# Kernel optimization log

Measured on AMD Instinct MI355X. Metric: run time of the kernel, lower is better.

## Reference

```python
import jax, jax.numpy as jnp
import numpy as np

N_HEAD = 16

def setup_inputs() -> dict:
    key = jax.random.key(0)
    k1, k2, k3 = jax.random.split(key, 3)
    B, T, C = 4, 2048, 1024
    x = jax.random.normal(k1, (B, T, C), dtype=jnp.float32)
    w_attn = jax.random.normal(k2, (C, 3 * C), dtype=jnp.float32) * (1.0 / np.sqrt(C))
    w_proj = jax.random.normal(k3, (C, C), dtype=jnp.float32) * (1.0 / np.sqrt(C))
    return {"x": x, "w_attn": w_attn, "w_proj": w_proj}

def reference(x, w_attn, w_proj):
    B, T, C = x.shape
    H = N_HEAD
    D = C // H
    qkv = x @ w_attn  # [B, T, 3C]
    q, k, v = jnp.split(qkv, 3, axis=2)
    # [B, H, T, D]
    q = q.reshape(B, T, H, D).transpose(0, 2, 1, 3)
    k = k.reshape(B, T, H, D).transpose(0, 2, 1, 3)
    v = v.reshape(B, T, H, D).transpose(0, 2, 1, 3)
    att = jnp.einsum('bhqd,bhkd->bhqk', q, k) * (1.0 / np.sqrt(D))
    causal = jnp.tril(jnp.ones((T, T), dtype=bool))
    att = jnp.where(causal[None, None, :, :], att, -jnp.inf)
    att = jax.nn.softmax(att, axis=-1)
    y = jnp.einsum('bhqk,bhkd->bhqd', att, v)  # [B, H, T, D]
    y = y.transpose(0, 2, 1, 3).reshape(B, T, C)
    return y @ w_proj
```

## Files before the change

### kernel.cpp

```cpp
#include <hip/hip_runtime.h>
#include <hip/hip_bf16.h>
#include <math.h>

#define B_   4
#define T_   2048
#define C_   1024
#define H_   16
#define D_   64
#define M_   (B_*T_)
#define N3   (3*C_)
#define KDIM C_

typedef __attribute__((ext_vector_type(8)))  short bf16x8;
typedef __attribute__((ext_vector_type(4)))  float f32x4;
typedef __attribute__((ext_vector_type(16))) float f32x16;
typedef __attribute__((ext_vector_type(4)))  unsigned int u32x4;

#define MFMA16(a,b,c) __builtin_amdgcn_mfma_f32_16x16x32_bf16(a,b,c,0,0,0)
#define MFMA32(a,b,c) __builtin_amdgcn_mfma_f32_32x32x16_bf16(a,b,c,0,0,0)

#define QSCALE 0.18033688011112042f

__device__ __forceinline__ unsigned short f2bf(float f) {
  union { float f; unsigned u; } a; a.f = f;
  unsigned r = a.u + 0x7fffu + ((a.u >> 16) & 1u);
  return (unsigned short)(r >> 16);
}

__device__ __forceinline__ unsigned cvtpk(float lo, float hi) {
  unsigned r;
  asm("v_cvt_pk_bf16_f32 %0, %1, %2" : "=v"(r) : "v"(lo), "v"(hi));
  return r;
}

__device__ __forceinline__ void gload16(const void* g, void* l) {
  __builtin_amdgcn_global_load_lds(
      (const __attribute__((address_space(1))) void*)g,
      (__attribute__((address_space(3))) void*)l, 16, 0, 0);
}

__global__ void cast_f32_bf16(const float* __restrict__ in,
                              unsigned short* __restrict__ out, int n) {
  int i = (blockIdx.x * 256 + threadIdx.x) * 4;
  if (i >= n) return;
  float4 v = *(const float4*)(in + i);
  ushort4 o;
  o.x = f2bf(v.x); o.y = f2bf(v.y); o.z = f2bf(v.z); o.w = f2bf(v.w);
  *(ushort4*)(out + i) = o;
}

__global__ void transpose_cast(const float* __restrict__ in,
                               unsigned short* __restrict__ out,
                               int R, int Ncols) {
  __shared__ float tile[32][33];
  int bc = blockIdx.x * 32;
  int br = blockIdx.y * 32;
  int tx = threadIdx.x, ty = threadIdx.y;
  #pragma unroll
  for (int i = ty; i < 32; i += 8)
    tile[i][tx] = in[(size_t)(br + i) * Ncols + bc + tx];
  __syncthreads();
  #pragma unroll
  for (int i = ty; i < 32; i += 8)
    out[(size_t)(bc + i) * R + br + tx] = f2bf(tile[tx][i]);
}

template<int MODE>
__global__ __launch_bounds__(256)
void gemm128(const unsigned short* __restrict__ A,
             const unsigned short* __restrict__ Bt,
             unsigned short* __restrict__ qo,
             unsigned short* __restrict__ ko,
             unsigned short* __restrict__ vto,
             float* __restrict__ outf) {
  __shared__ short Asl[128 * 64];
  __shared__ short Bsl[128 * 64];
  const int tid  = threadIdx.x;
  const int wid  = tid >> 6, lane = tid & 63;
  const int l15  = lane & 15, l4 = lane >> 4;
  const int tm   = blockIdx.y * 128;
  const int tn   = blockIdx.x * 128;
  const int wm   = (wid >> 1) * 64, wn = (wid & 1) * 64;

  f32x4 acc[4][4] = {};
  const int stoff = wid * 1024 + lane * 16;

  for (int kt = 0; kt < KDIM; kt += 64) {
    __syncthreads();
    #pragma unroll
    for (int ro = 0; ro < 4; ++ro) {
      int off = ro * 4096 + stoff;
      int row = off >> 7;
      int ce  = (off & 127) >> 1;
      gload16(A  + (size_t)(tm + row) * KDIM + kt + ce,
              (char*)Asl + ro * 4096 + wid * 1024);
      gload16(Bt + (size_t)(tn + row) * KDIM + kt + ce,
              (char*)Bsl + ro * 4096 + wid * 1024);
    }
    __syncthreads();

    #pragma unroll
    for (int ks = 0; ks < 2; ++ks) {
      bf16x8 af[4], bfr[4];
      #pragma unroll
      for (int i = 0; i < 4; ++i) {
        af[i]  = *(const bf16x8*)&Asl[(wm + i*16 + l15) * 64 + ks*32 + l4*8];
        bfr[i] = *(const bf16x8*)&Bsl[(wn + i*16 + l15) * 64 + ks*32 + l4*8];
      }
      #pragma unroll
      for (int mi = 0; mi < 4; ++mi)
        #pragma unroll
        for (int ni = 0; ni < 4; ++ni)
          acc[mi][ni] = MFMA16(af[mi], bfr[ni], acc[mi][ni]);
    }
  }

  #pragma unroll
  for (int mi = 0; mi < 4; ++mi) {
    #pragma unroll
    for (int ni = 0; ni < 4; ++ni) {
      #pragma unroll
      for (int r = 0; r < 4; ++r) {
        int m = tm + wm + mi*16 + l4*4 + r;
        int n = tn + wn + ni*16 + l15;
        float val = acc[mi][ni][r];
        if (MODE == 0) {
          int b = m >> 11, t = m & (T_ - 1);
          int which = n >> 10, n1 = n & (C_ - 1);
          int h = n1 >> 6, d = n1 & 63;
          size_t bh = (size_t)(b * H_ + h);
          if (which == 0)      qo[(bh * T_ + t) * D_ + d] = f2bf(val * QSCALE);
          else if (which == 1) ko[(bh * T_ + t) * D_ + d] = f2bf(val);
          else                 vto[(bh * D_ + d) * T_ + t] = f2bf(val);
        } else {
          outf[(size_t)m * C_ + n] = val;
        }
      }
    }
  }
}

__global__ __launch_bounds__(256)
void attn32(const unsigned short* __restrict__ Q,
            const unsigned short* __restrict__ K,
            const unsigned short* __restrict__ Vt,
            unsigned short* __restrict__ Y) {
  const int bh   = blockIdx.x;
  const int pair = blockIdx.y;
  const int lane = threadIdx.x & 63, w = threadIdx.x >> 6;
  const int l31  = lane & 31, hi = lane >> 5;
  const int b    = bh >> 4, h = bh & 15;

  const unsigned short* Qp = Q  + (size_t)bh * T_ * D_;
  const unsigned short* Kp = K  + (size_t)bh * T_ * D_;
  const unsigned short* Vp = Vt + (size_t)bh * D_ * T_;

  const int NQT = T_ / 128;

  for (int half = 0; half < 2; ++half) {
    const int qtile = half ? (NQT - 1 - pair) : pair;
    const int q0 = qtile * 128 + w * 32;

    bf16x8 qf[4];
    #pragma unroll
    for (int c = 0; c < 4; ++c)
      qf[c] = *(const bf16x8*)&Qp[(size_t)(q0 + l31) * D_ + c*16 + hi*8];

    f32x16 acc[2] = {};
    float m_q = -INFINITY, l_q = 0.f;

    const int nt = (q0 + 31) / 64 + 1;

    bf16x8 kfc[2][4];
    #pragma unroll
    for (int kb = 0; kb < 2; ++kb)
      #pragma unroll
      for (int c = 0; c < 4; ++c)
        kfc[kb][c] = *(const bf16x8*)&Kp[(size_t)(kb*32 + l31) * D_ + c*16 + hi*8];

    for (int kt = 0; kt < nt; ++kt) {
      const int k0 = kt * 64;

      f32x16 s2[2] = {};
      __builtin_amdgcn_s_setprio(1);
      #pragma unroll
      for (int c = 0; c < 4; ++c) s2[0] = MFMA32(kfc[0][c], qf[c], s2[0]);
      #pragma unroll
      for (int c = 0; c < 4; ++c) s2[1] = MFMA32(kfc[1][c], qf[c], s2[1]);
      __builtin_amdgcn_s_setprio(0);

      bf16x8 va[2][4];
      #pragma unroll
      for (int dt = 0; dt < 2; ++dt)
        #pragma unroll
        for (int s = 0; s < 4; ++s)
          va[dt][s] = *(const bf16x8*)&Vp[(size_t)(dt*32 + l31) * T_ + k0 + s*16 + hi*8];

      bf16x8 kfn[2][4];
      const bool havenext = (kt + 1 < nt);
      if (havenext) {
        const int k1 = k0 + 64;
        #pragma unroll
        for (int kb = 0; kb < 2; ++kb)
          #pragma unroll
          for (int c = 0; c < 4; ++c)
            kfn[kb][c] = *(const bf16x8*)&Kp[(size_t)(k1 + kb*32 + l31) * D_ + c*16 + hi*8];
      }

      if (kt == nt - 1) {
        #pragma unroll
        for (int kb = 0; kb < 2; ++kb)
          #pragma unroll
          for (int r = 0; r < 16; ++r) {
            int krow = k0 + kb*32 + (r&3) + 8*(r>>2) + 4*hi;
            if (krow > q0 + l31) s2[kb][r] = -INFINITY;
          }
      }

      float tmax = s2[0][0];
      #pragma unroll
      for (int kb = 0; kb < 2; ++kb)
        #pragma unroll
        for (int r = 0; r < 16; ++r) tmax = fmaxf(tmax, s2[kb][r]);

      if (!__all(tmax <= m_q + 8.0f)) {
        float tm2 = fmaxf(tmax, __shfl_xor(tmax, 32, 64));
        float mn  = fmaxf(m_q, tm2);
        float scale = exp2f(m_q - mn);
        m_q = mn;
        l_q *= scale;
        #pragma unroll
        for (int r = 0; r < 16; ++r) { acc[0][r] *= scale; acc[1][r] *= scale; }
      }

      float rsum = 0.f;
      #pragma unroll
      for (int kb = 0; kb < 2; ++kb)
        #pragma unroll
        for (int r = 0; r < 16; ++r) {
          float p = exp2f(s2[kb][r] - m_q);
          s2[kb][r] = p;
          rsum += p;
        }
      rsum += __shfl_xor(rsum, 32, 64);
      l_q += rsum;

      u32x4 pb[4];
      #pragma unroll
      for (int kb = 0; kb < 2; ++kb)
        #pragma unroll
        for (int ss = 0; ss < 2; ++ss)
          #pragma unroll
          for (int b2 = 0; b2 < 2; ++b2) {
            unsigned ce = cvtpk(s2[kb][8*ss     + 2*b2], s2[kb][8*ss     + 2*b2 + 1]);
            unsigned co = cvtpk(s2[kb][8*ss + 4 + 2*b2], s2[kb][8*ss + 4 + 2*b2 + 1]);
            auto rr = __builtin_amdgcn_permlane32_swap(ce, co, false, false);
            pb[kb*2 + ss][b2]     = rr[0];
            pb[kb*2 + ss][2 + b2] = rr[1];
          }

      __builtin_amdgcn_s_setprio(1);
      #pragma unroll
      for (int dt = 0; dt < 2; ++dt)
        #pragma unroll
        for (int s = 0; s < 4; ++s)
          acc[dt] = MFMA32(va[dt][s], __builtin_bit_cast(bf16x8, pb[s]), acc[dt]);
      __builtin_amdgcn_s_setprio(0);

      if (havenext) {
        #pragma unroll
        for (int kb = 0; kb < 2; ++kb)
          #pragma unroll
          for (int c = 0; c < 4; ++c)
            kfc[kb][c] = kfn[kb][c];
      }
    }

    float inv = 1.0f / l_q;
    const int t = q0 + l31;
    unsigned short* Yrow = Y + ((size_t)b * T_ + t) * C_ + h * D_;
    #pragma unroll
    for (int dt = 0; dt < 2; ++dt)
      #pragma unroll
      for (int rg = 0; rg < 4; ++rg) {
        uint2 wv;
        wv.x = cvtpk(acc[dt][rg*4 + 0] * inv, acc[dt][rg*4 + 1] * inv);
        wv.y = cvtpk(acc[dt][rg*4 + 2] * inv, acc[dt][rg*4 + 3] * inv);
        *(uint2*)(Yrow + dt*32 + rg*8 + hi*4) = wv;
      }
  }
}

extern "C" void kernel_launch(void* const* d_in, const int* in_sizes, int n_in,
                              void* d_out, int out_size, void* d_ws, size_t ws_size,
                              hipStream_t stream) {
  const float* x      = (const float*)d_in[0];
  const float* w_attn = (const float*)d_in[1];
  const float* w_proj = (const float*)d_in[2];
  float* out = (float*)d_out;

  char* ws = (char*)d_ws;
  size_t off = 0;
  auto alloc = [&](size_t bytes) {
    char* p = ws + off; off += (bytes + 255) & ~(size_t)255; return p;
  };
  unsigned short* xb  = (unsigned short*)alloc((size_t)M_ * C_ * 2);
  unsigned short* wat = (unsigned short*)alloc((size_t)N3 * KDIM * 2);
  unsigned short* wpt = (unsigned short*)alloc((size_t)C_ * C_ * 2);
  unsigned short* qb  = (unsigned short*)alloc((size_t)M_ * C_ * 2);
  unsigned short* kb  = (unsigned short*)alloc((size_t)M_ * C_ * 2);
  unsigned short* vtb = (unsigned short*)alloc((size_t)M_ * C_ * 2);
  unsigned short* yb  = (unsigned short*)alloc((size_t)M_ * C_ * 2);

  cast_f32_bf16<<<dim3(M_ * C_ / 1024), dim3(256), 0, stream>>>(x, xb, M_ * C_);
  transpose_cast<<<dim3(N3 / 32, KDIM / 32), dim3(32, 8), 0, stream>>>(w_attn, wat, KDIM, N3);
  transpose_cast<<<dim3(C_ / 32, C_ / 32), dim3(32, 8), 0, stream>>>(w_proj, wpt, C_, C_);

  gemm128<0><<<dim3(N3 / 128, M_ / 128), dim3(256), 0, stream>>>(xb, wat, qb, kb, vtb, nullptr);
  attn32<<<dim3(B_ * H_, T_ / 256), dim3(256), 0, stream>>>(qb, kb, vtb, yb);
  gemm128<1><<<dim3(C_ / 128, M_ / 128), dim3(256), 0, stream>>>(yb, wpt, nullptr, nullptr, nullptr, out);
}
```

Measured before the change: 351.6 us.

## Run both causal query tiles concurrently in 512-thread attention blocks

The attention kernel previously looped serially over a front and back query tile with 4 waves. It now launches 8 waves per block, with waves 0-3 taking tile p and waves 4-7 taking the mirrored tile 15-p, so both halves run concurrently. The loop is also restructured to load the next K tile directly into the current registers and to load V per d-half just before its MFMAs, cutting register pressure to fit launch_bounds(512,4). This raises parallelism and occupancy, but the two wave groups now finish at very different times inside one block, and the later V loads leave less latency hiding.

```diff
diff --git a/kernel.cpp b/kernel.cpp
--- a/kernel.cpp
+++ b/kernel.cpp
@@ -140,155 +140,139 @@
   }
 }
 
-__global__ __launch_bounds__(256)
+__global__ __launch_bounds__(512, 4)
 void attn32(const unsigned short* __restrict__ Q,
             const unsigned short* __restrict__ K,
             const unsigned short* __restrict__ Vt,
             unsigned short* __restrict__ Y) {
   const int bh   = blockIdx.x;
-  const int pair = blockIdx.y;
+  const int p    = blockIdx.y;
   const int lane = threadIdx.x & 63, w = threadIdx.x >> 6;
   const int l31  = lane & 31, hi = lane >> 5;
   const int b    = bh >> 4, h = bh & 15;
 
+  const int qtile = (w < 4) ? p : (15 - p);
+  const int q0    = qtile * 128 + (w & 3) * 32;
+
   const unsigned short* Qp = Q  + (size_t)bh * T_ * D_;
   const unsigned short* Kp = K  + (size_t)bh * T_ * D_;
   const unsigned short* Vp = Vt + (size_t)bh * D_ * T_;
 
-  const int NQT = T_ / 128;
-
-  for (int half = 0; half < 2; ++half) {
-    const int qtile = half ? (NQT - 1 - pair) : pair;
-    const int q0 = qtile * 128 + w * 32;
-
-    bf16x8 qf[4];
+  bf16x8 qf[4];
+  #pragma unroll
+  for (int c = 0; c < 4; ++c)
+    qf[c] = *(const bf16x8*)&Qp[(size_t)(q0 + l31) * D_ + c*16 + hi*8];
+
+  f32x16 acc[2] = {};
+  float m_q = -INFINITY, l_q = 0.f;
+
+  const int nt = (q0 + 31) / 64 + 1;
+
+  bf16x8 kfc[2][4];
+  #pragma unroll
+  for (int kb = 0; kb < 2; ++kb)
     #pragma unroll
     for (int c = 0; c < 4; ++c)
-      qf[c] = *(const bf16x8*)&Qp[(size_t)(q0 + l31) * D_ + c*16 + hi*8];
-
-    f32x16 acc[2] = {};
-    float m_q = -INFINITY, l_q = 0.f;
-
-    const int nt = (q0 + 31) / 64 + 1;
-
-    bf16x8 kfc[2][4];
-    #pragma unroll
-    for (int kb = 0; kb < 2; ++kb)
-      #pragma unroll
-      for (int c = 0; c < 4; ++c)
-        kfc[kb][c] = *(const bf16x8*)&Kp[(size_t)(kb*32 + l31) * D_ + c*16 + hi*8];
-
-    for (int kt = 0; kt < nt; ++kt) {
-      const int k0 = kt * 64;
-
-      f32x16 s2[2] = {};
-      __builtin_amdgcn_s_setprio(1);
-      #pragma unroll
-      for (int c = 0; c < 4; ++c) s2[0] = MFMA32(kfc[0][c], qf[c], s2[0]);
-      #pragma unroll
-      for (int c = 0; c < 4; ++c) s2[1] = MFMA32(kfc[1][c], qf[c], s2[1]);
-      __builtin_amdgcn_s_setprio(0);
-
-      bf16x8 va[2][4];
-      #pragma unroll
-      for (int dt = 0; dt < 2; ++dt)
-        #pragma unroll
-        for (int s = 0; s < 4; ++s)
-          va[dt][s] = *(const bf16x8*)&Vp[(size_t)(dt*32 + l31) * T_ + k0 + s*16 + hi*8];
-
-      bf16x8 kfn[2][4];
-      const bool havenext = (kt + 1 < nt);
-      if (havenext) {
-        const int k1 = k0 + 64;
-        #pragma unroll
-        for (int kb = 0; kb < 2; ++kb)
-          #pragma unroll
-          for (int c = 0; c < 4; ++c)
-            kfn[kb][c] = *(const bf16x8*)&Kp[(size_t)(k1 + kb*32 + l31) * D_ + c*16 + hi*8];
-      }
-
-      if (kt == nt - 1) {
-        #pragma unroll
-        for (int kb = 0; kb < 2; ++kb)
-          #pragma unroll
-          for (int r = 0; r < 16; ++r) {
-            int krow = k0 + kb*32 + (r&3) + 8*(r>>2) + 4*hi;
-            if (krow > q0 + l31) s2[kb][r] = -INFINITY;
-          }
-      }
-
-      float tmax = s2[0][0];
+      kfc[kb][c] = *(const bf16x8*)&Kp[(size_t)(kb*32 + l31) * D_ + c*16 + hi*8];
+
+  for (int kt = 0; kt < nt; ++kt) {
+    const int k0 = kt * 64;
+
+    f32x16 s2[2] = {};
+    __builtin_amdgcn_s_setprio(1);
+    #pragma unroll
+    for (int c = 0; c < 4; ++c) s2[0] = MFMA32(kfc[0][c], qf[c], s2[0]);
+    #pragma unroll
+    for (int c = 0; c < 4; ++c) s2[1] = MFMA32(kfc[1][c], qf[c], s2[1]);
+    __builtin_amdgcn_s_setprio(0);
+
+    if (kt + 1 < nt) {
+      const int k1 = k0 + 64;
       #pragma unroll
       for (int kb = 0; kb < 2; ++kb)
         #pragma unroll
-        for (int r = 0; r < 16; ++r) tmax = fmaxf(tmax, s2[kb][r]);
-
-      if (!__all(tmax <= m_q + 8.0f)) {
-        float tm2 = fmaxf(tmax, __shfl_xor(tmax, 32, 64));
-        float mn  = fmaxf(m_q, tm2);
-        float scale = exp2f(m_q - mn);
-        m_q = mn;
-        l_q *= scale;
-        #pragma unroll
-        for (int r = 0; r < 16; ++r) { acc[0][r] *= scale; acc[1][r] *= scale; }
-      }
-
-      float rsum = 0.f;
+        for (int c = 0; c < 4; ++c)
+          kfc[kb][c] = *(const bf16x8*)&Kp[(size_t)(k1 + kb*32 + l31) * D_ + c*16 + hi*8];
+    }
+
+    if (kt == nt - 1) {
       #pragma unroll
       for (int kb = 0; kb < 2; ++kb)
         #pragma unroll
         for (int r = 0; r < 16; ++r) {
-          float p = exp2f(s2[kb][r] - m_q);
-          s2[kb][r] = p;
-          rsum += p;
+          int krow = k0 + kb*32 + (r&3) + 8*(r>>2) + 4*hi;
+          if (krow > q0 + l31) s2[kb][r] = -INFINITY;
         }
-      rsum += __shfl_xor(rsum, 32, 64);
-      l_q += rsum;
-
-      u32x4 pb[4];
-      #pragma unroll
-      for (int kb = 0; kb < 2; ++kb)
+    }
+
+    float tmax = s2[0][0];
+    #pragma unroll
+    for (int kb = 0; kb < 2; ++kb)
+      #pragma unroll
+      for (int r = 0; r < 16; ++r) tmax = fmaxf(tmax, s2[kb][r]);
+
+    if (!__all(tmax <= m_q + 8.0f)) {
+      float tm2 = fmaxf(tmax, __shfl_xor(tmax, 32, 64));
+      float mn  = fmaxf(m_q, tm2);
+      float scale = exp2f(m_q - mn);
+      m_q = mn;
+      l_q *= scale;
+      #pragma unroll
+      for (int r = 0; r < 16; ++r) { acc[0][r] *= scale; acc[1][r] *= scale; }
+    }
+
+    float rsum = 0.f;
+    #pragma unroll
+    for (int kb = 0; kb < 2; ++kb)
+      #pragma unroll
+      for (int r = 0; r < 16; ++r) {
+        float pe = exp2f(s2[kb][r] - m_q);
+        s2[kb][r] = pe;
+        rsum += pe;
+      }
+    rsum += __shfl_xor(rsum, 32, 64);
+    l_q += rsum;
+
+    u32x4 pb[4];
+    #pragma unroll
+    for (int kb = 0; kb < 2; ++kb)
+      #pragma unroll
+      for (int ss = 0; ss < 2; ++ss)
         #pragma unroll
-        for (int ss = 0; ss < 2; ++ss)
-          #pragma unroll
-          for (int b2 = 0; b2 < 2; ++b2) {
-            unsigned ce = cvtpk(s2[kb][8*ss     + 2*b2], s2[kb][8*ss     + 2*b2 + 1]);
-            unsigned co = cvtpk(s2[kb][8*ss + 4 + 2*b2], s2[kb][8*ss + 4 + 2*b2 + 1]);
-            auto rr = __builtin_amdgcn_permlane32_swap(ce, co, false, false);
-            pb[kb*2 + ss][b2]     = rr[0];
-            pb[kb*2 + ss][2 + b2] = rr[1];
-          }
-
+        for (int b2 = 0; b2 < 2; ++b2) {
+          unsigned ce = cvtpk(s2[kb][8*ss     + 2*b2], s2[kb][8*ss     + 2*b2 + 1]);
+          unsigned co = cvtpk(s2[kb][8*ss + 4 + 2*b2], s2[kb][8*ss + 4 + 2*b2 + 1]);
+          auto rr = __builtin_amdgcn_permlane32_swap(ce, co, false, false);
+          pb[kb*2 + ss][b2]     = rr[0];
+          pb[kb*2 + ss][2 + b2] = rr[1];
+        }
+
+    #pragma unroll
+    for (int dt = 0; dt < 2; ++dt) {
+      bf16x8 va[4];
+      #pragma unroll
+      for (int s = 0; s < 4; ++s)
+        va[s] = *(const bf16x8*)&Vp[(size_t)(dt*32 + l31) * T_ + k0 + s*16 + hi*8];
       __builtin_amdgcn_s_setprio(1);
       #pragma unroll
-      for (int dt = 0; dt < 2; ++dt)
-        #pragma unroll
-        for (int s = 0; s < 4; ++s)
-          acc[dt] = MFMA32(va[dt][s], __builtin_bit_cast(bf16x8, pb[s]), acc[dt]);
+      for (int s = 0; s < 4; ++s)
+        acc[dt] = MFMA32(va[s], __builtin_bit_cast(bf16x8, pb[s]), acc[dt]);
       __builtin_amdgcn_s_setprio(0);
-
-      if (havenext) {
-        #pragma unroll
-        for (int kb = 0; kb < 2; ++kb)
-          #pragma unroll
-          for (int c = 0; c < 4; ++c)
-            kfc[kb][c] = kfn[kb][c];
-      }
-    }
-
-    float inv = 1.0f / l_q;
-    const int t = q0 + l31;
-    unsigned short* Yrow = Y + ((size_t)b * T_ + t) * C_ + h * D_;
-    #pragma unroll
-    for (int dt = 0; dt < 2; ++dt)
-      #pragma unroll
-      for (int rg = 0; rg < 4; ++rg) {
-        uint2 wv;
-        wv.x = cvtpk(acc[dt][rg*4 + 0] * inv, acc[dt][rg*4 + 1] * inv);
-        wv.y = cvtpk(acc[dt][rg*4 + 2] * inv, acc[dt][rg*4 + 3] * inv);
-        *(uint2*)(Yrow + dt*32 + rg*8 + hi*4) = wv;
-      }
+    }
   }
+
+  float inv = 1.0f / l_q;
+  const int t = q0 + l31;
+  unsigned short* Yrow = Y + ((size_t)b * T_ + t) * C_ + h * D_;
+  #pragma unroll
+  for (int dt = 0; dt < 2; ++dt)
+    #pragma unroll
+    for (int rg = 0; rg < 4; ++rg) {
+      uint2 wv;
+      wv.x = cvtpk(acc[dt][rg*4 + 0] * inv, acc[dt][rg*4 + 1] * inv);
+      wv.y = cvtpk(acc[dt][rg*4 + 2] * inv, acc[dt][rg*4 + 3] * inv);
+      *(uint2*)(Yrow + dt*32 + rg*8 + hi*4) = wv;
+    }
 }
 
 extern "C" void kernel_launch(void* const* d_in, const int* in_sizes, int n_in,
@@ -317,6 +301,6 @@
   transpose_cast<<<dim3(C_ / 32, C_ / 32), dim3(32, 8), 0, stream>>>(w_proj, wpt, C_, C_);
 
   gemm128<0><<<dim3(N3 / 128, M_ / 128), dim3(256), 0, stream>>>(xb, wat, qb, kb, vtb, nullptr);
-  attn32<<<dim3(B_ * H_, T_ / 256), dim3(256), 0, stream>>>(qb, kb, vtb, yb);
+  attn32<<<dim3(B_ * H_, 8), dim3(512), 0, stream>>>(qb, kb, vtb, yb);
   gemm128<1><<<dim3(C_ / 128, M_ / 128), dim3(256), 0, stream>>>(yb, wpt, nullptr, nullptr, nullptr, out);
 }
```

After: 384.1 us. +9.2%, slower.
